# Performance work log

Hardware: AMD Instinct MI355X
Metric: run time of the kernel (lower is better)

## Reference

```python
import jax, jax.numpy as jnp
import numpy as np

DIMINISH_FACTOR = 0.5  # init kwarg
MAX_DOC_LEN = 256
BATCH = 256


def setup_inputs() -> dict:
    key = jax.random.key(0)
    k1, k2, k3 = jax.random.split(key, 3)
    MM = MAX_DOC_LEN * MAX_DOC_LEN
    y_true = jax.random.randint(k1, (BATCH, MM, 2), 0, 2).astype(jnp.int32)
    y_pred = jax.random.uniform(k2, (BATCH, MM, 2), dtype=jnp.float32, minval=1e-6, maxval=1.0)
    doc_len = jax.random.randint(k3, (BATCH,), 1, MAX_DOC_LEN + 1).astype(jnp.int32)
    return {"y_true": y_true, "y_pred": y_pred, "doc_len": doc_len}


def reference(y_true, y_pred, doc_len) -> jnp.ndarray:
    B, MM, _ = y_pred.shape
    M = int(np.sqrt(MM))
    # getmask selects the top-left doc_len x doc_len block of the M x M pair grid.
    idx = jnp.arange(M, dtype=jnp.int32)
    dl = doc_len[:, None, None]
    valid = (idx[None, :, None] < dl) & (idx[None, None, :] < dl)  # [B, M, M]
    valid = valid.reshape(B, MM)
    logp = jnp.log(y_pred)  # [B, MM, 2]
    pos_mask = valid & (y_true[:, :, 1] == 1)
    neg_mask = valid & (y_true[:, :, 0] == 1)
    pos_loss = -jnp.sum(jnp.where(pos_mask, logp[:, :, 1], 0.0))
    neg_loss = -jnp.sum(jnp.where(neg_mask, logp[:, :, 0], 0.0))
    total = pos_loss + DIMINISH_FACTOR * neg_loss
    return total / jnp.sum(doc_len).astype(jnp.float32)
```

## Files before the change

kernel.cpp:

```cpp
#include <hip/hip_runtime.h>

#define MDIM 256
#define BATCH 256
#define DIMINISH 0.5f
#define ROWS_PER_BLOCK 16
#define BLOCKS_PER_BATCH (MDIM / ROWS_PER_BLOCK)
#define NBLOCKS (BATCH * BLOCKS_PER_BATCH)

__global__ __launch_bounds__(256) void row_loss_kernel(
    const int*   __restrict__ y_true,
    const float* __restrict__ y_pred,
    const int*   __restrict__ doc_len,
    float*       __restrict__ partial)
{
    const int blk  = blockIdx.x;
    const int b    = blk >> 4;
    const int r0   = (blk & 15) * ROWS_PER_BLOCK;
    const int dl   = doc_len[b];

    if (r0 >= dl) {
        if (threadIdx.x == 0) partial[blk] = 0.0f;
        return;
    }

    const int lane = threadIdx.x & 63;
    const int wid  = threadIdx.x >> 6;

    float sum = 0.0f;
    for (int r = r0 + wid; r < r0 + ROWS_PER_BLOCK; r += 4) {
        if (r >= dl) continue;
        const size_t rowbase = ((size_t)b * (MDIM * MDIM)) + (size_t)r * MDIM;
        #pragma unroll
        for (int c = 0; c < 2; ++c) {
            const int j = c * 128 + lane * 2;
            if (j >= dl) continue;
            const size_t e = (rowbase + (size_t)j) * 2;
            const int4   yt = *reinterpret_cast<const int4*>(y_true + e);
            const float4 yp = *reinterpret_cast<const float4*>(y_pred + e);
            sum -= (float)yt.y * __logf(yp.y) + DIMINISH * (float)yt.x * __logf(yp.x);
            if (j + 1 < dl)
                sum -= (float)yt.w * __logf(yp.w) + DIMINISH * (float)yt.z * __logf(yp.z);
        }
    }

    #pragma unroll
    for (int off = 32; off > 0; off >>= 1)
        sum += __shfl_down(sum, off, 64);

    __shared__ float wsum[4];
    if (lane == 0) wsum[wid] = sum;
    __syncthreads();
    if (threadIdx.x == 0)
        partial[blk] = wsum[0] + wsum[1] + wsum[2] + wsum[3];
}

__global__ __launch_bounds__(1024) void final_reduce_kernel(
    const float* __restrict__ partial,
    const int*   __restrict__ doc_len,
    float*       __restrict__ out)
{
    const int t    = threadIdx.x;
    const int lane = t & 63;
    const int wid  = t >> 6;

    float s = 0.0f;
    #pragma unroll
    for (int k = 0; k < NBLOCKS / 1024; ++k)
        s += partial[t + k * 1024];

    float d = (t < BATCH) ? (float)doc_len[t] : 0.0f;

    #pragma unroll
    for (int off = 32; off > 0; off >>= 1) {
        s += __shfl_down(s, off, 64);
        d += __shfl_down(d, off, 64);
    }

    __shared__ float wsum[16], wdl[16];
    if (lane == 0) { wsum[wid] = s; wdl[wid] = d; }
    __syncthreads();

    if (t < 64) {
        float v  = (t < 16) ? wsum[t] : 0.0f;
        float dv = (t < 16) ? wdl[t]  : 0.0f;
        #pragma unroll
        for (int off = 8; off > 0; off >>= 1) {
            v  += __shfl_down(v, off, 64);
            dv += __shfl_down(dv, off, 64);
        }
        if (t == 0) out[0] = v / dv;
    }
}

extern "C" void kernel_launch(void* const* d_in, const int* in_sizes, int n_in,
                              void* d_out, int out_size, void* d_ws, size_t ws_size,
                              hipStream_t stream)
{
    const int*   y_true  = (const int*)d_in[0];
    const float* y_pred  = (const float*)d_in[1];
    const int*   doc_len = (const int*)d_in[2];
    float*       out     = (float*)d_out;
    float*       partial = (float*)d_ws;

    row_loss_kernel<<<NBLOCKS, 256, 0, stream>>>(y_true, y_pred, doc_len, partial);
    final_reduce_kernel<<<1, 1024, 0, stream>>>(partial, doc_len, out);
}
```

Baseline: 26.90 us.

## Switch to grid-stride one-row-per-wave loop with 1024 persistent blocks

Replaces the 4096-block launch (16 rows per block) with 1024 blocks whose waves stride over all 65536 rows, one row per wave per iteration, each lane covering four columns with two 16-byte loads per input. Valid columns are selected with a multiply by 0 or 1 instead of branches, and the final reduce now reads one partial per thread. The aim is to balance the triangular valid-region work across the machine and cut block launch overhead. In exchange, every wave reads doc_len for each row and walks rows that are skipped, and consecutive rows interleave across waves.

```diff
diff --git a/kernel.cpp b/kernel.cpp
--- a/kernel.cpp
+++ b/kernel.cpp
@@ -2,56 +2,58 @@
 
 #define MDIM 256
 #define BATCH 256
+#define NROWS (BATCH * MDIM)
 #define DIMINISH 0.5f
-#define ROWS_PER_BLOCK 16
-#define BLOCKS_PER_BATCH (MDIM / ROWS_PER_BLOCK)
-#define NBLOCKS (BATCH * BLOCKS_PER_BATCH)
+#define NBLK 1024
+#define NTHR 256
+#define WAVES_PER_BLK (NTHR / 64)
+#define NWAVES (NBLK * WAVES_PER_BLK)
 
-__global__ __launch_bounds__(256) void row_loss_kernel(
+__global__ __launch_bounds__(NTHR) void row_loss_kernel(
     const int*   __restrict__ y_true,
     const float* __restrict__ y_pred,
     const int*   __restrict__ doc_len,
     float*       __restrict__ partial)
 {
-    const int blk  = blockIdx.x;
-    const int b    = blk >> 4;
-    const int r0   = (blk & 15) * ROWS_PER_BLOCK;
-    const int dl   = doc_len[b];
-
-    if (r0 >= dl) {
-        if (threadIdx.x == 0) partial[blk] = 0.0f;
-        return;
-    }
-
     const int lane = threadIdx.x & 63;
     const int wid  = threadIdx.x >> 6;
+    const int gw   = blockIdx.x * WAVES_PER_BLK + wid;
+    const int j0   = lane * 4;
 
     float sum = 0.0f;
-    for (int r = r0 + wid; r < r0 + ROWS_PER_BLOCK; r += 4) {
-        if (r >= dl) continue;
-        const size_t rowbase = ((size_t)b * (MDIM * MDIM)) + (size_t)r * MDIM;
-        #pragma unroll
-        for (int c = 0; c < 2; ++c) {
-            const int j = c * 128 + lane * 2;
-            if (j >= dl) continue;
-            const size_t e = (rowbase + (size_t)j) * 2;
-            const int4   yt = *reinterpret_cast<const int4*>(y_true + e);
-            const float4 yp = *reinterpret_cast<const float4*>(y_pred + e);
-            sum -= (float)yt.y * __logf(yp.y) + DIMINISH * (float)yt.x * __logf(yp.x);
-            if (j + 1 < dl)
-                sum -= (float)yt.w * __logf(yp.w) + DIMINISH * (float)yt.z * __logf(yp.z);
-        }
+    for (int rid = gw; rid < NROWS; rid += NWAVES) {
+        const int b  = rid >> 8;
+        const int i  = rid & 255;
+        const int dl = doc_len[b];
+        if (i >= dl || j0 >= dl) continue;
+
+        const size_t e = ((size_t)rid * MDIM + (size_t)j0) * 2;
+        const int4   t0 = *reinterpret_cast<const int4*>(y_true + e);
+        const int4   t1 = *reinterpret_cast<const int4*>(y_true + e + 4);
+        const float4 p0 = *reinterpret_cast<const float4*>(y_pred + e);
+        const float4 p1 = *reinterpret_cast<const float4*>(y_pred + e + 4);
+
+        float s = 0.0f;
+        s += ((j0 + 0) < dl ? 1.0f : 0.0f) *
+             ((float)t0.y * __logf(p0.y) + DIMINISH * (float)t0.x * __logf(p0.x));
+        s += ((j0 + 1) < dl ? 1.0f : 0.0f) *
+             ((float)t0.w * __logf(p0.w) + DIMINISH * (float)t0.z * __logf(p0.z));
+        s += ((j0 + 2) < dl ? 1.0f : 0.0f) *
+             ((float)t1.y * __logf(p1.y) + DIMINISH * (float)t1.x * __logf(p1.x));
+        s += ((j0 + 3) < dl ? 1.0f : 0.0f) *
+             ((float)t1.w * __logf(p1.w) + DIMINISH * (float)t1.z * __logf(p1.z));
+        sum -= s;
     }
 
     #pragma unroll
     for (int off = 32; off > 0; off >>= 1)
         sum += __shfl_down(sum, off, 64);
 
-    __shared__ float wsum[4];
+    __shared__ float wsum[WAVES_PER_BLK];
     if (lane == 0) wsum[wid] = sum;
     __syncthreads();
     if (threadIdx.x == 0)
-        partial[blk] = wsum[0] + wsum[1] + wsum[2] + wsum[3];
+        partial[blockIdx.x] = wsum[0] + wsum[1] + wsum[2] + wsum[3];
 }
 
 __global__ __launch_bounds__(1024) void final_reduce_kernel(
@@ -63,11 +65,7 @@
     const int lane = t & 63;
     const int wid  = t >> 6;
 
-    float s = 0.0f;
-    #pragma unroll
-    for (int k = 0; k < NBLOCKS / 1024; ++k)
-        s += partial[t + k * 1024];
-
+    float s = partial[t];
     float d = (t < BATCH) ? (float)doc_len[t] : 0.0f;
 
     #pragma unroll
@@ -102,6 +100,6 @@
     float*       out     = (float*)d_out;
     float*       partial = (float*)d_ws;
 
-    row_loss_kernel<<<NBLOCKS, 256, 0, stream>>>(y_true, y_pred, doc_len, partial);
+    row_loss_kernel<<<NBLK, NTHR, 0, stream>>>(y_true, y_pred, doc_len, partial);
     final_reduce_kernel<<<1, 1024, 0, stream>>>(partial, doc_len, out);
 }
```

Result: slower. 28.88 us (+7.4%).
